# Optimization experiments

Measured on AMD Instinct MI355X. Metric: run time of the kernel, lower is better.

Reference implementation:

```python
import jax, jax.numpy as jnp
import numpy as np

N_IN, N_OUT = 1152, 10          # input/output capsule counts
D_IN, D_OUT = 8, 16             # input/output capsule dims
NUM_ROUTING = 3
BATCH = 256
EPS = 1e-9


def squash(s, axis=-1):
    # squash(s) = (|s|^2 / (1 + |s|^2)) * s / |s|
    sq = jnp.sum(s * s, axis=axis, keepdims=True)
    return (sq / (1.0 + sq)) * s / jnp.sqrt(sq + EPS)


def setup_inputs() -> dict:
    key = jax.random.key(0)
    kx, kw = jax.random.split(key)
    x = jax.random.normal(kx, (BATCH, D_IN, N_IN), dtype=jnp.float32)
    weight = jax.random.normal(kw, (N_IN, N_OUT, D_OUT, D_IN), dtype=jnp.float32)
    return {"x": x, "weight": weight}


def reference(x, weight):
    # u_hat[b,i,j,:] = W[i,j] @ x[b,:,i]   -> [B, N_IN, N_OUT, D_OUT]
    u_hat = jnp.einsum('ijod,bdi->bijo', weight, x)
    # routing logits b_ij shared across the batch (fully bipartite capsule graph)
    b = jnp.zeros((N_IN, N_OUT), dtype=x.dtype)
    v = None
    for _ in range(NUM_ROUTING):
        c = jax.nn.softmax(b, axis=1)                       # coupling over output caps j
        s = jnp.einsum('ij,bijo->bjo', c, u_hat)            # weighted sum of predictions
        v = squash(s)                                       # [B, N_OUT, D_OUT]
        # agreement: <u_hat, v>, averaged over batch (as in the DGL example)
        b = b + jnp.mean(jnp.einsum('bijo,bjo->bij', u_hat, v), axis=0)
    return v
```

## Files before the change

### kernel.cpp

```cpp
#include <hip/hip_runtime.h>

#define B_     256
#define NI_    1152
#define NO_    10
#define DO_    16
#define DI_    8
#define PAIRS_ 160
#define SEGS_  128
#define ISEG_  (NI_/SEGS_)
#define PP_    5


__global__ __launch_bounds__(256) void prep_kernel(const float* __restrict__ x,
                                                   float* __restrict__ xT,
                                                   float* __restrict__ blog,
                                                   float* __restrict__ cmat)
{
    int vb = blockIdx.x;
    int tid = threadIdx.x, lane = tid & 63, wv = tid >> 6;
    if (vb < 576) {
        __shared__ float tile[64 * 65];
        int d = vb & 7, rest = vb >> 3, tb = rest & 3, ti = rest >> 2;
        int i0 = ti * 64, b0 = tb * 64;
#pragma unroll
        for (int k = 0; k < 16; ++k) {
            int bL = wv * 16 + k;
            tile[bL * 65 + lane] = x[(size_t)(b0 + bL) * (NI_ * DI_) + d * NI_ + i0 + lane];
        }
        __syncthreads();
#pragma unroll
        for (int k = 0; k < 16; ++k) {
            int iL = wv * 16 + k;
            xT[((size_t)(i0 + iL) * DI_ + d) * B_ + b0 + lane] = tile[lane * 65 + iL];
        }
    } else {
        int g = (vb - 576) * 256 + tid;
        if (g < NI_ * NO_) { blog[g] = 0.f; cmat[g] = 0.1f; }
    }
}

__global__ __launch_bounds__(256, 4) void sv_kernel(const float* __restrict__ xT,
                                                    const float* __restrict__ W,
                                                    const float* __restrict__ cmat,
                                                    float* __restrict__ partial)
{
    int ps   = blockIdx.x;
    int seg  = blockIdx.y;
    int tid  = threadIdx.x;
    int lane = tid & 63;
    int wv   = __builtin_amdgcn_readfirstlane(tid >> 6);
    int p0   = ps * (4 * PP_) + wv * PP_;
    int b0   = lane * 4;
    int i0   = seg * ISEG_;

    float acc[PP_][4];
#pragma unroll
    for (int p = 0; p < PP_; ++p)
#pragma unroll
        for (int r = 0; r < 4; ++r) acc[p][r] = 0.f;

    float4 nx[DI_];
#pragma unroll
    for (int d = 0; d < DI_; ++d)
        nx[d] = *(const float4*)&xT[((size_t)i0 * DI_ + d) * B_ + b0];

    for (int ii = 0; ii < ISEG_; ++ii) {
        int i = i0 + ii;
        float4 cx[DI_];
#pragma unroll
        for (int d = 0; d < DI_; ++d) cx[d] = nx[d];
        if (ii + 1 < ISEG_) {
#pragma unroll
            for (int d = 0; d < DI_; ++d)
                nx[d] = *(const float4*)&xT[((size_t)(i + 1) * DI_ + d) * B_ + b0];
        }
        const float* __restrict__ crow = cmat + i * NO_;
        const float* __restrict__ wb   = W + (size_t)(i * PAIRS_ + p0) * DI_;
#pragma unroll
        for (int p = 0; p < PP_; ++p) {
            const float* wr = wb + p * DI_;
            float cv = crow[(p0 + p) >> 4];
            float u0 = wr[0] * cx[0].x, u1 = wr[0] * cx[0].y;
            float u2 = wr[0] * cx[0].z, u3 = wr[0] * cx[0].w;
#pragma unroll
            for (int d = 1; d < DI_; ++d) {
                u0 = fmaf(wr[d], (&cx[d].x)[0], u0);
                u1 = fmaf(wr[d], (&cx[d].x)[1], u1);
                u2 = fmaf(wr[d], (&cx[d].x)[2], u2);
                u3 = fmaf(wr[d], (&cx[d].x)[3], u3);
            }
            acc[p][0] = fmaf(cv, u0, acc[p][0]);
            acc[p][1] = fmaf(cv, u1, acc[p][1]);
            acc[p][2] = fmaf(cv, u2, acc[p][2]);
            acc[p][3] = fmaf(cv, u3, acc[p][3]);
        }
    }
#pragma unroll
    for (int p = 0; p < PP_; ++p)
        *(float4*)&partial[(size_t)(seg * PAIRS_ + p0 + p) * B_ + b0] =
            make_float4(acc[p][0], acc[p][1], acc[p][2], acc[p][3]);
}

__global__ __launch_bounds__(256) void red_kernel(const float* __restrict__ partial,
                                                  float* __restrict__ vbuf,
                                                  float* __restrict__ out,
                                                  int write_out)
{
    int j   = blockIdx.x;
    int bc  = blockIdx.y;
    int o   = threadIdx.x >> 4;
    int b_l = threadIdx.x & 15;
    int b   = bc * 16 + b_l;
    int pair = j * DO_ + o;

    float s = 0.f;
    for (int seg = 0; seg < SEGS_; ++seg)
        s += partial[(size_t)(seg * PAIRS_ + pair) * B_ + b];

    __shared__ float so[DO_][17];
    so[o][b_l] = s;
    __syncthreads();
    float sq = 0.f;
#pragma unroll
    for (int oo = 0; oo < DO_; ++oo) { float t = so[oo][b_l]; sq = fmaf(t, t, sq); }
    float f = (sq / (1.f + sq)) * rsqrtf(sq + 1e-9f);
    float vv = s * f;
    vbuf[pair * B_ + b] = vv;
    if (write_out) out[(size_t)b * PAIRS_ + pair] = vv;
}

__global__ __launch_bounds__(256) void agree_kernel(const float* __restrict__ xT,
                                                    const float* __restrict__ W,
                                                    const float* __restrict__ vbuf,
                                                    float* __restrict__ blog,
                                                    float* __restrict__ cmat)
{
    int i    = blockIdx.x;
    int lane = threadIdx.x & 63;
    int wv   = __builtin_amdgcn_readfirstlane(threadIdx.x >> 6);
    int b0   = lane * 4;

    float xv[DI_][4];
#pragma unroll
    for (int d = 0; d < DI_; ++d) {
        float4 t4 = *(const float4*)&xT[((size_t)i * DI_ + d) * B_ + b0];
        xv[d][0] = t4.x; xv[d][1] = t4.y; xv[d][2] = t4.z; xv[d][3] = t4.w;
    }
    __shared__ float js[NO_];
    __shared__ float nbs[NO_];
    for (int j = wv; j < NO_; j += 4) {
        const float* __restrict__ wj = W + (size_t)(i * NO_ + j) * DO_ * DI_;
        float aj = 0.f;
#pragma unroll
        for (int o = 0; o < DO_; ++o) {
            const float* wr = wj + o * DI_;
            float4 vv4 = *(const float4*)&vbuf[(j * DO_ + o) * B_ + b0];
            float u0 = wr[0] * xv[0][0], u1 = wr[0] * xv[0][1];
            float u2 = wr[0] * xv[0][2], u3 = wr[0] * xv[0][3];
#pragma unroll
            for (int d = 1; d < DI_; ++d) {
                u0 = fmaf(wr[d], xv[d][0], u0); u1 = fmaf(wr[d], xv[d][1], u1);
                u2 = fmaf(wr[d], xv[d][2], u2); u3 = fmaf(wr[d], xv[d][3], u3);
            }
            aj = fmaf(u0, vv4.x, aj); aj = fmaf(u1, vv4.y, aj);
            aj = fmaf(u2, vv4.z, aj); aj = fmaf(u3, vv4.w, aj);
        }
        for (int off = 32; off > 0; off >>= 1) aj += __shfl_down(aj, off);
        if (lane == 0) js[j] = aj;
    }
    __syncthreads();
    if (threadIdx.x < NO_) {
        float nb = blog[i * NO_ + threadIdx.x] + js[threadIdx.x] * (1.f / B_);
        blog[i * NO_ + threadIdx.x] = nb;
        nbs[threadIdx.x] = nb;
    }
    __syncthreads();
    if (threadIdx.x < NO_) {
        float m = nbs[0];
#pragma unroll
        for (int k = 1; k < NO_; ++k) m = fmaxf(m, nbs[k]);
        float ssum = 0.f;
#pragma unroll
        for (int k = 0; k < NO_; ++k) ssum += __expf(nbs[k] - m);
        cmat[i * NO_ + threadIdx.x] = __expf(nbs[threadIdx.x] - m) / ssum;
    }
}


__global__ __launch_bounds__(256) void c_old(float* __restrict__ blog,
                                             float* __restrict__ cmat, int init)
{
    int i = blockIdx.x * 256 + threadIdx.x;
    if (i >= NI_) return;
    if (init) {
#pragma unroll
        for (int j = 0; j < NO_; ++j) { cmat[i * NO_ + j] = 0.1f; blog[i * NO_ + j] = 0.f; }
        return;
    }
    float r[NO_]; float m = -1e30f;
#pragma unroll
    for (int j = 0; j < NO_; ++j) { r[j] = blog[i * NO_ + j]; m = fmaxf(m, r[j]); }
    float s = 0.f;
#pragma unroll
    for (int j = 0; j < NO_; ++j) { r[j] = __expf(r[j] - m); s += r[j]; }
    float inv = 1.f / s;
#pragma unroll
    for (int j = 0; j < NO_; ++j) cmat[i * NO_ + j] = r[j] * inv;
}

__global__ __launch_bounds__(640) void sv_old(const float* __restrict__ x,
                                              const float* __restrict__ W,
                                              const float* __restrict__ cmat,
                                              float* __restrict__ vbuf,
                                              float* __restrict__ out, int write_out)
{
    __shared__ __align__(16) float xL[NI_ * DI_];
    __shared__ float sred[4 * PAIRS_];
    __shared__ float sfin[PAIRS_];
    int b = blockIdx.x;
    {
        const float4* xs = (const float4*)(x + (size_t)b * NI_ * DI_);
        for (int t = threadIdx.x; t < NI_ * DI_ / 4; t += 640) {
            float4 v4 = xs[t];
            int f = 4 * t; int d = f / NI_; int i = f - d * NI_;
            xL[i * DI_ + d] = v4.x; xL[(i+1) * DI_ + d] = v4.y;
            xL[(i+2) * DI_ + d] = v4.z; xL[(i+3) * DI_ + d] = v4.w;
        }
    }
    __syncthreads();
    int pair = threadIdx.x % PAIRS_;
    int seg  = threadIdx.x / PAIRS_;
    int j    = pair >> 4;
    const float4* Wq = (const float4*)W;
    float acc = 0.f;
    int i0 = seg * (NI_ / 4);
    for (int i = i0; i < i0 + NI_ / 4; ++i) {
        float4 w0 = Wq[(i * PAIRS_ + pair) * 2];
        float4 w1 = Wq[(i * PAIRS_ + pair) * 2 + 1];
        const float* xp = &xL[i * DI_];
        float u = w0.x * xp[0] + w0.y * xp[1] + w0.z * xp[2] + w0.w * xp[3]
                + w1.x * xp[4] + w1.y * xp[5] + w1.z * xp[6] + w1.w * xp[7];
        acc = fmaf(cmat[i * NO_ + j], u, acc);
    }
    sred[threadIdx.x] = acc;
    __syncthreads();
    float s = 0.f;
    if (threadIdx.x < PAIRS_) {
        s = sred[threadIdx.x] + sred[PAIRS_ + threadIdx.x]
          + sred[2 * PAIRS_ + threadIdx.x] + sred[3 * PAIRS_ + threadIdx.x];
        sfin[threadIdx.x] = s;
    }
    __syncthreads();
    if (threadIdx.x < PAIRS_) {
        int jj = threadIdx.x >> 4;
        float sq = 0.f;
#pragma unroll
        for (int o = 0; o < DO_; ++o) { float t = sfin[(jj << 4) + o]; sq = fmaf(t, t, sq); }
        float vv = s * (sq / (1.f + sq)) * rsqrtf(sq + 1e-9f);
        vbuf[b * PAIRS_ + threadIdx.x] = vv;
        if (write_out) out[b * PAIRS_ + threadIdx.x] = vv;
    }
}

__global__ __launch_bounds__(256) void agree_old(const float* __restrict__ x,
                                                 const float* __restrict__ W,
                                                 const float* __restrict__ vbuf,
                                                 float* __restrict__ blog)
{
    int i = blockIdx.x;
    int b = threadIdx.x;
    float xr[DI_];
#pragma unroll
    for (int d = 0; d < DI_; ++d) xr[d] = x[((size_t)b * DI_ + d) * NI_ + i];
    __shared__ float red[4][NO_];
    int lane = threadIdx.x & 63;
    int wv   = threadIdx.x >> 6;
    for (int j = 0; j < NO_; ++j) {
        const float* vp = &vbuf[b * PAIRS_ + j * DO_];
        float aj = 0.f;
#pragma unroll
        for (int o = 0; o < DO_; ++o) {
            const float* wr = W + (size_t)((i * NO_ + j) * DO_ + o) * DI_;
            float u = wr[0] * xr[0] + wr[1] * xr[1] + wr[2] * xr[2] + wr[3] * xr[3]
                    + wr[4] * xr[4] + wr[5] * xr[5] + wr[6] * xr[6] + wr[7] * xr[7];
            aj = fmaf(u, vp[o], aj);
        }
        float val = aj;
        for (int off = 32; off > 0; off >>= 1) val += __shfl_down(val, off);
        if (lane == 0) red[wv][j] = val;
    }
    __syncthreads();
    if (threadIdx.x < NO_) {
        float sum = red[0][threadIdx.x] + red[1][threadIdx.x]
                  + red[2][threadIdx.x] + red[3][threadIdx.x];
        blog[i * NO_ + threadIdx.x] += sum * (1.f / B_);
    }
}


extern "C" void kernel_launch(void* const* d_in, const int* in_sizes, int n_in,
                              void* d_out, int out_size, void* d_ws, size_t ws_size,
                              hipStream_t stream)
{
    const float* x = (const float*)d_in[0];
    const float* W = (const float*)d_in[1];
    float* out = (float*)d_out;

    const size_t XT_N  = (size_t)NI_ * DI_ * B_;
    const size_t LOG_N = NI_ * NO_;
    const size_t V_N   = PAIRS_ * B_;
    const size_t P_N   = (size_t)SEGS_ * PAIRS_ * B_;
    const size_t NEED  = (XT_N + 2 * LOG_N + V_N + P_N) * sizeof(float);

    if (ws_size >= NEED) {
        float* xT      = (float*)d_ws;
        float* blog    = xT + XT_N;
        float* cmat    = blog + LOG_N;
        float* vbuf    = cmat + LOG_N;
        float* partial = vbuf + V_N;

        prep_kernel<<<576 + 45, 256, 0, stream>>>(x, xT, blog, cmat);
        for (int it = 0; it < 3; ++it) {
            sv_kernel<<<dim3(8, SEGS_), 256, 0, stream>>>(xT, W, cmat, partial);
            red_kernel<<<dim3(NO_, B_ / 16), 256, 0, stream>>>(partial, vbuf, out,
                                                               it == 2 ? 1 : 0);
            if (it < 2) agree_kernel<<<NI_, 256, 0, stream>>>(xT, W, vbuf, blog, cmat);
        }
    } else {
        float* blog = (float*)d_ws;
        float* cmat = blog + LOG_N;
        float* vbuf = cmat + LOG_N;
        for (int it = 0; it < 3; ++it) {
            c_old<<<(NI_ + 255) / 256, 256, 0, stream>>>(blog, cmat, it == 0 ? 1 : 0);
            sv_old<<<B_, 640, 0, stream>>>(x, W, cmat, vbuf, out, it == 2 ? 1 : 0);
            if (it < 2) agree_old<<<NI_, 256, 0, stream>>>(x, W, vbuf, blog);
        }
    }
}
```

Measured before the change: 184.9 us.

## Widen per-wave pair tiles in sv_kernel and process two input capsules per agree block

sv_kernel now gives each wave 10 output pairs instead of 5, halving the grid to 128x4 blocks. The grid axes are swapped, the inner i loop is fully unrolled, and occupancy is lowered to 2 blocks per SM, so each xT load is reused across more FMAs. agree_kernel handles two input capsules per block, sharing each vbuf load between them, and its grid is halved. The risks are higher register pressure and fewer blocks in flight, which may reduce latency hiding.

After: 275.4 us. +48.9%, slower.

```diff
diff --git a/kernel.cpp b/kernel.cpp
--- a/kernel.cpp
+++ b/kernel.cpp
@@ -8,7 +8,8 @@
 #define PAIRS_ 160
 #define SEGS_  128
 #define ISEG_  (NI_/SEGS_)
-#define PP_    5
+#define PSV_   4
+#define PPW_   10
 
 
 __global__ __launch_bounds__(256) void prep_kernel(const float* __restrict__ x,
@@ -39,23 +40,23 @@
     }
 }
 
-__global__ __launch_bounds__(256, 4) void sv_kernel(const float* __restrict__ xT,
+__global__ __launch_bounds__(256, 2) void sv_kernel(const float* __restrict__ xT,
                                                     const float* __restrict__ W,
                                                     const float* __restrict__ cmat,
                                                     float* __restrict__ partial)
 {
-    int ps   = blockIdx.x;
-    int seg  = blockIdx.y;
+    int seg  = blockIdx.x;
+    int ps   = blockIdx.y;
     int tid  = threadIdx.x;
     int lane = tid & 63;
     int wv   = __builtin_amdgcn_readfirstlane(tid >> 6);
-    int p0   = ps * (4 * PP_) + wv * PP_;
+    int p0   = ps * (4 * PPW_) + wv * PPW_;
     int b0   = lane * 4;
     int i0   = seg * ISEG_;
 
-    float acc[PP_][4];
-#pragma unroll
-    for (int p = 0; p < PP_; ++p)
+    float acc[PPW_][4];
+#pragma unroll
+    for (int p = 0; p < PPW_; ++p)
 #pragma unroll
         for (int r = 0; r < 4; ++r) acc[p][r] = 0.f;
 
@@ -64,6 +65,7 @@
     for (int d = 0; d < DI_; ++d)
         nx[d] = *(const float4*)&xT[((size_t)i0 * DI_ + d) * B_ + b0];
 
+#pragma unroll
     for (int ii = 0; ii < ISEG_; ++ii) {
         int i = i0 + ii;
         float4 cx[DI_];
@@ -77,7 +79,7 @@
         const float* __restrict__ crow = cmat + i * NO_;
         const float* __restrict__ wb   = W + (size_t)(i * PAIRS_ + p0) * DI_;
 #pragma unroll
-        for (int p = 0; p < PP_; ++p) {
+        for (int p = 0; p < PPW_; ++p) {
             const float* wr = wb + p * DI_;
             float cv = crow[(p0 + p) >> 4];
             float u0 = wr[0] * cx[0].x, u1 = wr[0] * cx[0].y;
@@ -96,7 +98,7 @@
         }
     }
 #pragma unroll
-    for (int p = 0; p < PP_; ++p)
+    for (int p = 0; p < PPW_; ++p)
         *(float4*)&partial[(size_t)(seg * PAIRS_ + p0 + p) * B_ + b0] =
             make_float4(acc[p][0], acc[p][1], acc[p][2], acc[p][3]);
 }
@@ -129,60 +131,75 @@
     if (write_out) out[(size_t)b * PAIRS_ + pair] = vv;
 }
 
-__global__ __launch_bounds__(256) void agree_kernel(const float* __restrict__ xT,
-                                                    const float* __restrict__ W,
-                                                    const float* __restrict__ vbuf,
-                                                    float* __restrict__ blog,
-                                                    float* __restrict__ cmat)
-{
-    int i    = blockIdx.x;
+__global__ __launch_bounds__(256, 2) void agree_kernel(const float* __restrict__ xT,
+                                                       const float* __restrict__ W,
+                                                       const float* __restrict__ vbuf,
+                                                       float* __restrict__ blog,
+                                                       float* __restrict__ cmat)
+{
+    int i0   = blockIdx.x * 2;
     int lane = threadIdx.x & 63;
     int wv   = __builtin_amdgcn_readfirstlane(threadIdx.x >> 6);
     int b0   = lane * 4;
 
-    float xv[DI_][4];
+    float xv0[DI_][4], xv1[DI_][4];
 #pragma unroll
     for (int d = 0; d < DI_; ++d) {
-        float4 t4 = *(const float4*)&xT[((size_t)i * DI_ + d) * B_ + b0];
-        xv[d][0] = t4.x; xv[d][1] = t4.y; xv[d][2] = t4.z; xv[d][3] = t4.w;
-    }
-    __shared__ float js[NO_];
-    __shared__ float nbs[NO_];
+        float4 a = *(const float4*)&xT[((size_t)i0 * DI_ + d) * B_ + b0];
+        float4 c = *(const float4*)&xT[((size_t)(i0 + 1) * DI_ + d) * B_ + b0];
+        xv0[d][0] = a.x; xv0[d][1] = a.y; xv0[d][2] = a.z; xv0[d][3] = a.w;
+        xv1[d][0] = c.x; xv1[d][1] = c.y; xv1[d][2] = c.z; xv1[d][3] = c.w;
+    }
+    __shared__ float js[2][NO_];
+    __shared__ float nbs[2][NO_];
     for (int j = wv; j < NO_; j += 4) {
-        const float* __restrict__ wj = W + (size_t)(i * NO_ + j) * DO_ * DI_;
-        float aj = 0.f;
+        const float* __restrict__ wj0 = W + (size_t)(i0 * NO_ + j) * DO_ * DI_;
+        const float* __restrict__ wj1 = W + (size_t)((i0 + 1) * NO_ + j) * DO_ * DI_;
+        float aj0 = 0.f, aj1 = 0.f;
 #pragma unroll
         for (int o = 0; o < DO_; ++o) {
-            const float* wr = wj + o * DI_;
+            const float* wr0 = wj0 + o * DI_;
+            const float* wr1 = wj1 + o * DI_;
             float4 vv4 = *(const float4*)&vbuf[(j * DO_ + o) * B_ + b0];
-            float u0 = wr[0] * xv[0][0], u1 = wr[0] * xv[0][1];
-            float u2 = wr[0] * xv[0][2], u3 = wr[0] * xv[0][3];
+            float u0 = wr0[0] * xv0[0][0], u1 = wr0[0] * xv0[0][1];
+            float u2 = wr0[0] * xv0[0][2], u3 = wr0[0] * xv0[0][3];
+            float w0 = wr1[0] * xv1[0][0], w1 = wr1[0] * xv1[0][1];
+            float w2 = wr1[0] * xv1[0][2], w3 = wr1[0] * xv1[0][3];
 #pragma unroll
             for (int d = 1; d < DI_; ++d) {
-                u0 = fmaf(wr[d], xv[d][0], u0); u1 = fmaf(wr[d], xv[d][1], u1);
-                u2 = fmaf(wr[d], xv[d][2], u2); u3 = fmaf(wr[d], xv[d][3], u3);
+                u0 = fmaf(wr0[d], xv0[d][0], u0); u1 = fmaf(wr0[d], xv0[d][1], u1);
+                u2 = fmaf(wr0[d], xv0[d][2], u2); u3 = fmaf(wr0[d], xv0[d][3], u3);
+                w0 = fmaf(wr1[d], xv1[d][0], w0); w1 = fmaf(wr1[d], xv1[d][1], w1);
+                w2 = fmaf(wr1[d], xv1[d][2], w2); w3 = fmaf(wr1[d], xv1[d][3], w3);
             }
-            aj = fmaf(u0, vv4.x, aj); aj = fmaf(u1, vv4.y, aj);
-            aj = fmaf(u2, vv4.z, aj); aj = fmaf(u3, vv4.w, aj);
-        }
-        for (int off = 32; off > 0; off >>= 1) aj += __shfl_down(aj, off);
-        if (lane == 0) js[j] = aj;
-    }
-    __syncthreads();
-    if (threadIdx.x < NO_) {
-        float nb = blog[i * NO_ + threadIdx.x] + js[threadIdx.x] * (1.f / B_);
-        blog[i * NO_ + threadIdx.x] = nb;
-        nbs[threadIdx.x] = nb;
-    }
-    __syncthreads();
-    if (threadIdx.x < NO_) {
-        float m = nbs[0];
-#pragma unroll
-        for (int k = 1; k < NO_; ++k) m = fmaxf(m, nbs[k]);
+            aj0 = fmaf(u0, vv4.x, aj0); aj0 = fmaf(u1, vv4.y, aj0);
+            aj0 = fmaf(u2, vv4.z, aj0); aj0 = fmaf(u3, vv4.w, aj0);
+            aj1 = fmaf(w0, vv4.x, aj1); aj1 = fmaf(w1, vv4.y, aj1);
+            aj1 = fmaf(w2, vv4.z, aj1); aj1 = fmaf(w3, vv4.w, aj1);
+        }
+        for (int off = 32; off > 0; off >>= 1) {
+            aj0 += __shfl_down(aj0, off);
+            aj1 += __shfl_down(aj1, off);
+        }
+        if (lane == 0) { js[0][j] = aj0; js[1][j] = aj1; }
+    }
+    __syncthreads();
+    if (threadIdx.x < 2 * NO_) {
+        int ii = threadIdx.x / NO_, j = threadIdx.x % NO_;
+        float nb = blog[(i0 + ii) * NO_ + j] + js[ii][j] * (1.f / B_);
+        blog[(i0 + ii) * NO_ + j] = nb;
+        nbs[ii][j] = nb;
+    }
+    __syncthreads();
+    if (threadIdx.x < 2 * NO_) {
+        int ii = threadIdx.x / NO_, j = threadIdx.x % NO_;
+        float m = nbs[ii][0];
+#pragma unroll
+        for (int k = 1; k < NO_; ++k) m = fmaxf(m, nbs[ii][k]);
         float ssum = 0.f;
 #pragma unroll
-        for (int k = 0; k < NO_; ++k) ssum += __expf(nbs[k] - m);
-        cmat[i * NO_ + threadIdx.x] = __expf(nbs[threadIdx.x] - m) / ssum;
+        for (int k = 0; k < NO_; ++k) ssum += __expf(nbs[ii][k] - m);
+        cmat[(i0 + ii) * NO_ + j] = __expf(nbs[ii][j] - m) / ssum;
     }
 }
 
@@ -321,10 +338,10 @@
 
         prep_kernel<<<576 + 45, 256, 0, stream>>>(x, xT, blog, cmat);
         for (int it = 0; it < 3; ++it) {
-            sv_kernel<<<dim3(8, SEGS_), 256, 0, stream>>>(xT, W, cmat, partial);
+            sv_kernel<<<dim3(SEGS_, PSV_), 256, 0, stream>>>(xT, W, cmat, partial);
             red_kernel<<<dim3(NO_, B_ / 16), 256, 0, stream>>>(partial, vbuf, out,
                                                                it == 2 ? 1 : 0);
-            if (it < 2) agree_kernel<<<NI_, 256, 0, stream>>>(xT, W, vbuf, blog, cmat);
+            if (it < 2) agree_kernel<<<NI_ / 2, 256, 0, stream>>>(xT, W, vbuf, blog, cmat);
         }
     } else {
         float* blog = (float*)d_ws;
```
